# Kernel optimization log

Hardware: AMD Instinct MI355X
Metric: run time of the kernel (lower is better)

## Reference

```python
import jax, jax.numpy as jnp
import numpy as np

B, T, XS, HS = 256, 512, 256, 256


def setup_inputs() -> dict:
    key = jax.random.key(0)
    ks = jax.random.split(key, 9)
    scale_x = np.sqrt(6.0 / (XS + HS)).astype(np.float32)  # xavier_uniform-like scale
    scale_h = np.sqrt(6.0 / (HS + HS)).astype(np.float32)
    d = {"x": jax.random.normal(ks[0], (B, T, XS), dtype=jnp.float32)}
    names = ["i", "f", "g", "o"]
    for n, kx, kh in zip(names, ks[1:5], ks[5:9]):
        d[f"wx_{n}"] = jax.random.uniform(kx, (XS, HS), jnp.float32, -scale_x, scale_x)
        d[f"wh_{n}"] = jax.random.uniform(kh, (HS, HS), jnp.float32, -scale_h, scale_h)
        d[f"bx_{n}"] = jnp.zeros((HS,), jnp.float32)
        d[f"bh_{n}"] = jnp.zeros((HS,), jnp.float32)
    return d


def reference(x, wx_i, bx_i, wh_i, bh_i, wx_f, bx_f, wh_f, bh_f,
              wx_g, bx_g, wh_g, bh_g, wx_o, bx_o, wh_o, bh_o):
    bs, ts, xs = x.shape
    hs = wx_i.shape[1]
    # Fuse the 4 input projections and 4 hidden projections into 2 GEMMs
    # (identical math to 8 separate matmuls).
    Wx = jnp.concatenate([wx_i, wx_f, wx_g, wx_o], axis=1)      # [xs, 4hs]
    Wh = jnp.concatenate([wh_i, wh_f, wh_g, wh_o], axis=1)      # [hs, 4hs]
    b = jnp.concatenate([bx_i + bh_i, bx_f + bh_f, bx_g + bh_g, bx_o + bh_o])

    # Precompute all input projections in one big GEMM: [bs, ts, 4hs]
    x_proj = jnp.einsum('btx,xg->btg', x, Wx) + b

    def step(carry, xt_proj):
        h, c = carry
        gates = xt_proj + h @ Wh                      # [bs, 4hs]
        i_t = jax.nn.sigmoid(gates[:, 0 * hs:1 * hs])
        f_t = jax.nn.sigmoid(gates[:, 1 * hs:2 * hs])
        g_t = jnp.tanh(gates[:, 2 * hs:3 * hs])
        o_t = jax.nn.sigmoid(gates[:, 3 * hs:4 * hs])
        c_new = f_t * c + i_t * g_t
        h_new = o_t * jnp.tanh(c_new)
        return (h_new, c_new), None

    h0 = jnp.zeros((bs, hs), x.dtype)
    c0 = jnp.zeros((bs, hs), x.dtype)
    (h_t, c_t), _ = jax.lax.scan(step, (h0, c0), jnp.swapaxes(x_proj, 0, 1))
    return (h_t, c_t)
```

## Files before the change

### kernel.cpp

```cpp
#include <hip/hip_runtime.h>
#include <hip/hip_bf16.h>

#define BB   256
#define TT   512
#define XSZ  256
#define HSZ  256
#define GLDSW 132

typedef __bf16 bf16_t;
typedef __attribute__((ext_vector_type(8))) __bf16 bf16x8;
typedef __attribute__((ext_vector_type(4))) float  f32x4;
typedef __attribute__((ext_vector_type(4))) unsigned uint4v;

__device__ __forceinline__ float sigmoidf_(float v) { return 1.0f / (1.0f + __expf(-v)); }
__device__ __forceinline__ float tanhf_(float v)    { return 1.0f - 2.0f / (1.0f + __expf(2.0f * v)); }

__global__ void prep_bias(const float* bx0, const float* bh0, const float* bx1, const float* bh1,
                          const float* bx2, const float* bh2, const float* bx3, const float* bh3,
                          float* bias) {
  const float* bxs[4] = {bx0, bx1, bx2, bx3};
  const float* bhs[4] = {bh0, bh1, bh2, bh3};
  int g = blockIdx.x, c = threadIdx.x;
  bias[g * 256 + c] = bxs[g][c] + bhs[g][c];
}

__global__ void prep_wtf(const float* wx0, const float* wh0, const float* wx1, const float* wh1,
                         const float* wx2, const float* wh2, const float* wx3, const float* wh3,
                         bf16_t* Wtf) {
  const float* whs[4] = {wh0, wh1, wh2, wh3};
  const float* wxs[4] = {wx0, wx1, wx2, wx3};
  int id = blockIdx.x * 256 + threadIdx.x;
  int L  = id & 63;
  int kt = (id >> 6) & 15;
  int w  = (id >> 10) & 7;
  int j  = (id >> 13) & 7;
  int sec = w >> 1, half = w & 1;
  int c   = j * 32 + half * 16 + (L & 15);
  int k0  = kt * 32 + (L >> 4) * 8;
  const float* src = (k0 < 256) ? (whs[sec] + (size_t)k0 * 256 + c)
                                : (wxs[sec] + (size_t)(k0 - 256) * 256 + c);
  bf16x8 v;
#pragma unroll
  for (int i = 0; i < 8; ++i) v[i] = (__bf16)src[(size_t)i * 256];
  reinterpret_cast<bf16x8*>(Wtf)[id] = v;
}

__global__ void prep_xbf(const float* __restrict__ x, bf16_t* __restrict__ xb) {
  size_t id = (size_t)blockIdx.x * 256 + threadIdx.x;
  const float* p = x + id * 8;
  f32x4 lo = *reinterpret_cast<const f32x4*>(p);
  f32x4 hi = *reinterpret_cast<const f32x4*>(p + 4);
  bf16x8 v;
#pragma unroll
  for (int i = 0; i < 4; ++i) { v[i] = (__bf16)lo[i]; v[i + 4] = (__bf16)hi[i]; }
  reinterpret_cast<bf16x8*>(xb)[id] = v;
}

template <bool XBF>
__global__ __launch_bounds__(512, 2)
void lstm_seq(const void* __restrict__ xsrc, const bf16_t* __restrict__ Wtf,
              const float* __restrict__ bias, unsigned* __restrict__ hseq,
              float* __restrict__ out)
{
  __shared__ __align__(16) char  bxlds[65536];
  __shared__ __align__(16) char  hxl[2][8192];
  __shared__ __align__(16) float glds[16 * GLDSW];

  const int tid  = threadIdx.x;
  const int w    = tid >> 6;
  const int lane = tid & 63;
  const int l15  = lane & 15, l4 = lane >> 4;
  const int bid  = blockIdx.x;
  const int g    = bid >> 3, j = bid & 7;
  const int b0   = g * 16;
  const int sec  = w >> 1, half = w & 1;
  const int C    = sec * 256 + j * 32 + half * 16 + l15;

  const float*  xf32 = (const float*)xsrc;
  const bf16_t* xbf  = (const bf16_t*)xsrc;

  const float bias_v = bias[C];

  const char* wbase = (const char*)Wtf + ((size_t)(j * 8 + w) * 16) * 1024 + lane * 16;
  bf16x8 Bh[8];
#pragma unroll
  for (int kt = 0; kt < 8; ++kt)
    Bh[kt] = *reinterpret_cast<const bf16x8*>(wbase + kt * 1024);
#pragma unroll
  for (int q = 0; q < 8; ++q) {
    bf16x8 v = *reinterpret_cast<const bf16x8*>(wbase + (8 + q) * 1024);
    *reinterpret_cast<bf16x8*>(bxlds + (w * 8 + q) * 1024 + lane * 16) = v;
  }
  __syncthreads();

  const int crow = tid >> 5;
  const int ccol = tid & 31;
  float cst = 0.f;

  f32x4 acc_x = {bias_v, bias_v, bias_v, bias_v};
#pragma unroll
  for (int k8 = 0; k8 < 8; ++k8) {
    bf16x8 a;
    if constexpr (XBF) {
      a = *reinterpret_cast<const bf16x8*>(
          xbf + (size_t)(b0 + l15) * (TT * XSZ) + k8 * 32 + l4 * 8);
    } else {
      const float* xp = xf32 + (size_t)(b0 + l15) * (TT * XSZ) + k8 * 32 + l4 * 8;
      f32x4 lo = *reinterpret_cast<const f32x4*>(xp);
      f32x4 hi = *reinterpret_cast<const f32x4*>(xp + 4);
#pragma unroll
      for (int i = 0; i < 4; ++i) { a[i] = (__bf16)lo[i]; a[i + 4] = (__bf16)hi[i]; }
    }
    bf16x8 bx = *reinterpret_cast<const bf16x8*>(bxlds + (w * 8 + k8) * 1024 + lane * 16);
    acc_x = __builtin_amdgcn_mfma_f32_16x16x32_bf16(a, bx, acc_x, 0, 0, 0);
  }

#pragma unroll 1
  for (int t = 0; t < TT; ++t) {
    f32x4 acc = acc_x;

    bf16x8 ax[8];
    if constexpr (XBF) {
      if (t + 1 < TT) {
#pragma unroll
        for (int k8 = 0; k8 < 8; ++k8)
          ax[k8] = *reinterpret_cast<const bf16x8*>(
              xbf + (size_t)(b0 + l15) * (TT * XSZ) + (size_t)(t + 1) * XSZ + k8 * 32 + l4 * 8);
      }
    }

    if (t > 0) {
      const unsigned* hp = hseq + (size_t)(t & 1) * 65536
                         + (size_t)(b0 + l15) * HSZ + w * 32 + l4 * 8;
      const unsigned tg = (unsigned)t;
      uint4v A, B;
      for (;;) {
        asm volatile("global_load_dwordx4 %0, %2, off sc0 sc1\n\t"
                     "global_load_dwordx4 %1, %2, off offset:16 sc0 sc1\n\t"
                     "s_waitcnt vmcnt(0)"
                     : "=&v"(A), "=&v"(B) : "v"(hp) : "memory");
        bool ok = ((A[0] >> 16) == tg) & ((A[1] >> 16) == tg) &
                  ((A[2] >> 16) == tg) & ((A[3] >> 16) == tg) &
                  ((B[0] >> 16) == tg) & ((B[1] >> 16) == tg) &
                  ((B[2] >> 16) == tg) & ((B[3] >> 16) == tg);
        if (__all((int)ok)) break;
        __builtin_amdgcn_s_sleep(1);
      }
      __builtin_amdgcn_sched_barrier(0);
      unsigned p0 = (A[0] & 0xFFFFu) | (A[1] << 16);
      unsigned p1 = (A[2] & 0xFFFFu) | (A[3] << 16);
      unsigned p2 = (B[0] & 0xFFFFu) | (B[1] << 16);
      unsigned p3 = (B[2] & 0xFFFFu) | (B[3] << 16);
      uint4v pk = {p0, p1, p2, p3};
      *reinterpret_cast<uint4v*>(hxl[t & 1] + w * 1024 + lane * 16) = pk;
    }
    __syncthreads();

    if (t > 0) {
#pragma unroll
      for (int kt = 0; kt < 8; ++kt) {
        bf16x8 a = *reinterpret_cast<const bf16x8*>(hxl[t & 1] + kt * 1024 + lane * 16);
        acc = __builtin_amdgcn_mfma_f32_16x16x32_bf16(a, Bh[kt], acc, 0, 0, 0);
      }
    }

    {
      const int col = sec * 32 + half * 16 + l15;
#pragma unroll
      for (int r = 0; r < 4; ++r)
        glds[(l4 * 4 + r) * GLDSW + col] = acc[r];
    }
    __syncthreads();

    const float* gp = &glds[crow * GLDSW + ccol];
    float i_t = sigmoidf_(gp[0]);
    float f_t = sigmoidf_(gp[32]);
    float g_t = tanhf_(gp[64]);
    float o_t = sigmoidf_(gp[96]);
    float cn  = f_t * cst + i_t * g_t;
    cst = cn;
    float hval = o_t * tanhf_(cn);

    if (t + 1 < TT) {
      __bf16 hb16 = (__bf16)hval;
      unsigned hv = ((unsigned)(t + 1) << 16)
                  | (unsigned)__builtin_bit_cast(unsigned short, hb16);
      unsigned* hp = hseq + (size_t)((t + 1) & 1) * 65536
                   + (size_t)(b0 + crow) * HSZ + j * 32 + ccol;
      asm volatile("global_store_dword %0, %1, off sc0 sc1" :: "v"(hp), "v"(hv) : "memory");

      acc_x = f32x4{bias_v, bias_v, bias_v, bias_v};
#pragma unroll
      for (int k8 = 0; k8 < 8; ++k8) {
        bf16x8 a;
        if constexpr (XBF) {
          a = ax[k8];
        } else {
          const float* xp = xf32 + (size_t)(b0 + l15) * (TT * XSZ)
                          + (size_t)(t + 1) * XSZ + k8 * 32 + l4 * 8;
          f32x4 lo = *reinterpret_cast<const f32x4*>(xp);
          f32x4 hi = *reinterpret_cast<const f32x4*>(xp + 4);
#pragma unroll
          for (int i = 0; i < 4; ++i) { a[i] = (__bf16)lo[i]; a[i + 4] = (__bf16)hi[i]; }
        }
        bf16x8 bx = *reinterpret_cast<const bf16x8*>(bxlds + (w * 8 + k8) * 1024 + lane * 16);
        acc_x = __builtin_amdgcn_mfma_f32_16x16x32_bf16(a, bx, acc_x, 0, 0, 0);
      }
    } else {
      float* op = out + (size_t)(b0 + crow) * HSZ + j * 32 + ccol;
      op[0] = hval;
      op[(size_t)BB * HSZ] = cst;
    }
  }
}

extern "C" void kernel_launch(void* const* d_in, const int* in_sizes, int n_in,
                              void* d_out, int out_size, void* d_ws, size_t ws_size,
                              hipStream_t stream) {
  const float* x = (const float*)d_in[0];
  const float *wx[4], *wh[4], *bx[4], *bh[4];
  for (int g = 0; g < 4; ++g) {
    wx[g] = (const float*)d_in[1 + 4 * g];
    wh[g] = (const float*)d_in[2 + 4 * g];
    bx[g] = (const float*)d_in[3 + 4 * g];
    bh[g] = (const float*)d_in[4 + 4 * g];
  }

  char* ws = (char*)d_ws;
  float*    bias = (float*)ws;
  bf16_t*   Wtf  = (bf16_t*)(ws + 4096);
  unsigned* hseq = (unsigned*)(ws + 4096 + 1048576);
  bf16_t*   xbf  = (bf16_t*)(ws + 4096 + 1048576 + 524288);
  const size_t need_xbf = 4096 + 1048576 + 524288 + (size_t)BB * TT * XSZ * 2;

  prep_bias<<<dim3(4), dim3(256), 0, stream>>>(bx[0], bh[0], bx[1], bh[1],
                                               bx[2], bh[2], bx[3], bh[3], bias);
  prep_wtf<<<dim3(256), dim3(256), 0, stream>>>(wx[0], wh[0], wx[1], wh[1],
                                                wx[2], wh[2], wx[3], wh[3], Wtf);
  if (ws_size >= need_xbf) {
    prep_xbf<<<dim3((BB * TT * XSZ / 8) / 256), dim3(256), 0, stream>>>(x, xbf);
    lstm_seq<true><<<dim3(128), dim3(512), 0, stream>>>(xbf, Wtf, bias, hseq,
                                                        (float*)d_out);
  } else {
    lstm_seq<false><<<dim3(128), dim3(512), 0, stream>>>(x, Wtf, bias, hseq,
                                                         (float*)d_out);
  }
}
```

Baseline: 1.861 ms.

## Interleave gate columns so cell update runs in registers via lane shuffles

Reorders the fused weight layout so each group of four adjacent MFMA output columns holds the i/f/g/o gates of one hidden unit. The gate combination and cell update then run directly from the accumulators using lane shuffles, removing the LDS gate staging buffer and one block-wide barrier per timestep. Each wave now computes two N-tiles with all Wh and Wx fragments held in registers, so the grid halves to 64 blocks and the LDS copy of Wx goes away. The trade-offs are much higher register pressure, fewer blocks taking part in the recurrence, and the dropped prefetch of the next x step.

After: 2.227 ms. 1.2x slower.

```diff
diff --git a/kernel.cpp b/kernel.cpp
--- a/kernel.cpp
+++ b/kernel.cpp
@@ -5,15 +5,13 @@
 #define TT   512
 #define XSZ  256
 #define HSZ  256
-#define GLDSW 132
 
 typedef __bf16 bf16_t;
 typedef __attribute__((ext_vector_type(8))) __bf16 bf16x8;
 typedef __attribute__((ext_vector_type(4))) float  f32x4;
 typedef __attribute__((ext_vector_type(4))) unsigned uint4v;
 
-__device__ __forceinline__ float sigmoidf_(float v) { return 1.0f / (1.0f + __expf(-v)); }
-__device__ __forceinline__ float tanhf_(float v)    { return 1.0f - 2.0f / (1.0f + __expf(2.0f * v)); }
+__device__ __forceinline__ f32x4 splat4(float v) { f32x4 r = {v, v, v, v}; return r; }
 
 __global__ void prep_bias(const float* bx0, const float* bh0, const float* bx1, const float* bh1,
                           const float* bx2, const float* bh2, const float* bx3, const float* bh3,
@@ -32,13 +30,15 @@
   int id = blockIdx.x * 256 + threadIdx.x;
   int L  = id & 63;
   int kt = (id >> 6) & 15;
-  int w  = (id >> 10) & 7;
-  int j  = (id >> 13) & 7;
-  int sec = w >> 1, half = w & 1;
-  int c   = j * 32 + half * 16 + (L & 15);
-  int k0  = kt * 32 + (L >> 4) * 8;
-  const float* src = (k0 < 256) ? (whs[sec] + (size_t)k0 * 256 + c)
-                                : (wxs[sec] + (size_t)(k0 - 256) * 256 + c);
+  int nt = (id >> 10) & 1;
+  int w  = (id >> 11) & 7;
+  int j  = (id >> 14) & 3;
+  int tc   = L & 15;
+  int gate = tc & 3;
+  int hc   = j * 64 + w * 8 + nt * 4 + (tc >> 2);
+  int k0   = kt * 32 + (L >> 4) * 8;
+  const float* src = (k0 < 256) ? (whs[gate] + (size_t)k0 * 256 + hc)
+                                : (wxs[gate] + (size_t)(k0 - 256) * 256 + hc);
   bf16x8 v;
 #pragma unroll
   for (int i = 0; i < 8; ++i) v[i] = (__bf16)src[(size_t)i * 256];
@@ -62,42 +62,42 @@
               const float* __restrict__ bias, unsigned* __restrict__ hseq,
               float* __restrict__ out)
 {
-  __shared__ __align__(16) char  bxlds[65536];
-  __shared__ __align__(16) char  hxl[2][8192];
-  __shared__ __align__(16) float glds[16 * GLDSW];
+  __shared__ __align__(16) char hxl[2][8192];
 
   const int tid  = threadIdx.x;
   const int w    = tid >> 6;
   const int lane = tid & 63;
   const int l15  = lane & 15, l4 = lane >> 4;
   const int bid  = blockIdx.x;
-  const int g    = bid >> 3, j = bid & 7;
+  const int g    = bid >> 2, j = bid & 3;
   const int b0   = g * 16;
-  const int sec  = w >> 1, half = w & 1;
-  const int C    = sec * 256 + j * 32 + half * 16 + l15;
+  const int gate = l15 & 3;
+  const int hcg  = l15 >> 2;
+  const bool isg = (gate == 2);
 
   const float*  xf32 = (const float*)xsrc;
   const bf16_t* xbf  = (const bf16_t*)xsrc;
 
-  const float bias_v = bias[C];
-
-  const char* wbase = (const char*)Wtf + ((size_t)(j * 8 + w) * 16) * 1024 + lane * 16;
-  bf16x8 Bh[8];
-#pragma unroll
-  for (int kt = 0; kt < 8; ++kt)
-    Bh[kt] = *reinterpret_cast<const bf16x8*>(wbase + kt * 1024);
-#pragma unroll
-  for (int q = 0; q < 8; ++q) {
-    bf16x8 v = *reinterpret_cast<const bf16x8*>(wbase + (8 + q) * 1024);
-    *reinterpret_cast<bf16x8*>(bxlds + (w * 8 + q) * 1024 + lane * 16) = v;
-  }
-  __syncthreads();
-
-  const int crow = tid >> 5;
-  const int ccol = tid & 31;
-  float cst = 0.f;
-
-  f32x4 acc_x = {bias_v, bias_v, bias_v, bias_v};
+  const char* wbase = (const char*)Wtf + (size_t)(j * 256 + w * 32) * 1024 + lane * 16;
+  bf16x8 Bh[2][8], Bx[2][8];
+#pragma unroll
+  for (int nt = 0; nt < 2; ++nt)
+#pragma unroll
+    for (int kt = 0; kt < 8; ++kt) {
+      Bh[nt][kt] = *reinterpret_cast<const bf16x8*>(wbase + (nt * 16 + kt) * 1024);
+      Bx[nt][kt] = *reinterpret_cast<const bf16x8*>(wbase + (nt * 16 + 8 + kt) * 1024);
+    }
+
+  float bias_v[2];
+#pragma unroll
+  for (int nt = 0; nt < 2; ++nt)
+    bias_v[nt] = bias[gate * 256 + j * 64 + w * 8 + nt * 4 + hcg];
+
+  f32x4 cst0 = {0.f, 0.f, 0.f, 0.f};
+  f32x4 cst1 = {0.f, 0.f, 0.f, 0.f};
+
+  f32x4 acc_x0 = splat4(bias_v[0]);
+  f32x4 acc_x1 = splat4(bias_v[1]);
 #pragma unroll
   for (int k8 = 0; k8 < 8; ++k8) {
     bf16x8 a;
@@ -111,23 +111,14 @@
 #pragma unroll
       for (int i = 0; i < 4; ++i) { a[i] = (__bf16)lo[i]; a[i + 4] = (__bf16)hi[i]; }
     }
-    bf16x8 bx = *reinterpret_cast<const bf16x8*>(bxlds + (w * 8 + k8) * 1024 + lane * 16);
-    acc_x = __builtin_amdgcn_mfma_f32_16x16x32_bf16(a, bx, acc_x, 0, 0, 0);
+    acc_x0 = __builtin_amdgcn_mfma_f32_16x16x32_bf16(a, Bx[0][k8], acc_x0, 0, 0, 0);
+    acc_x1 = __builtin_amdgcn_mfma_f32_16x16x32_bf16(a, Bx[1][k8], acc_x1, 0, 0, 0);
   }
 
 #pragma unroll 1
   for (int t = 0; t < TT; ++t) {
-    f32x4 acc = acc_x;
-
-    bf16x8 ax[8];
-    if constexpr (XBF) {
-      if (t + 1 < TT) {
-#pragma unroll
-        for (int k8 = 0; k8 < 8; ++k8)
-          ax[k8] = *reinterpret_cast<const bf16x8*>(
-              xbf + (size_t)(b0 + l15) * (TT * XSZ) + (size_t)(t + 1) * XSZ + k8 * 32 + l4 * 8);
-      }
-    }
+    f32x4 acc0 = acc_x0;
+    f32x4 acc1 = acc_x1;
 
     if (t > 0) {
       const unsigned* hp = hseq + (size_t)(t & 1) * 65536
@@ -160,41 +151,72 @@
 #pragma unroll
       for (int kt = 0; kt < 8; ++kt) {
         bf16x8 a = *reinterpret_cast<const bf16x8*>(hxl[t & 1] + kt * 1024 + lane * 16);
-        acc = __builtin_amdgcn_mfma_f32_16x16x32_bf16(a, Bh[kt], acc, 0, 0, 0);
-      }
-    }
-
-    {
-      const int col = sec * 32 + half * 16 + l15;
-#pragma unroll
-      for (int r = 0; r < 4; ++r)
-        glds[(l4 * 4 + r) * GLDSW + col] = acc[r];
-    }
-    __syncthreads();
-
-    const float* gp = &glds[crow * GLDSW + ccol];
-    float i_t = sigmoidf_(gp[0]);
-    float f_t = sigmoidf_(gp[32]);
-    float g_t = tanhf_(gp[64]);
-    float o_t = sigmoidf_(gp[96]);
-    float cn  = f_t * cst + i_t * g_t;
-    cst = cn;
-    float hval = o_t * tanhf_(cn);
+        acc0 = __builtin_amdgcn_mfma_f32_16x16x32_bf16(a, Bh[0][kt], acc0, 0, 0, 0);
+        acc1 = __builtin_amdgcn_mfma_f32_16x16x32_bf16(a, Bh[1][kt], acc1, 0, 0, 0);
+      }
+    }
+
+    float hsel[2], csel[2];
+#pragma unroll
+    for (int nt = 0; nt < 2; ++nt) {
+      f32x4 acc = nt ? acc1 : acc0;
+      f32x4 av;
+#pragma unroll
+      for (int r = 0; r < 4; ++r) {
+        float p = isg ? 2.f * acc[r] : acc[r];
+        float s = 1.f / (1.f + __expf(-p));
+        av[r] = isg ? (2.f * s - 1.f) : s;
+      }
+      f32x4 bv, v0, v1, c0, c1;
+#pragma unroll
+      for (int r = 0; r < 4; ++r) bv[r] = __shfl_xor(av[r], 1);
+#pragma unroll
+      for (int r = 0; r < 4; ++r) {
+        v0[r] = (gate & 1) ? bv[r] : av[r];
+        v1[r] = (gate & 1) ? av[r] : bv[r];
+      }
+#pragma unroll
+      for (int r = 0; r < 4; ++r) { c0[r] = __shfl_xor(v0[r], 2); c1[r] = __shfl_xor(v1[r], 2); }
+      f32x4 hv;
+      f32x4 cs = nt ? cst1 : cst0;
+#pragma unroll
+      for (int r = 0; r < 4; ++r) {
+        float iv = (gate & 2) ? c0[r] : v0[r];
+        float fv = (gate & 2) ? c1[r] : v1[r];
+        float gv = (gate & 2) ? v0[r] : c0[r];
+        float ov = (gate & 2) ? v1[r] : c1[r];
+        float cn = fv * cs[r] + iv * gv;
+        cs[r] = cn;
+        float s2 = 1.f / (1.f + __expf(-2.f * cn));
+        hv[r] = ov * (2.f * s2 - 1.f);
+      }
+      if (nt) cst1 = cs; else cst0 = cs;
+      float hs = (gate == 0) ? hv[0] : (gate == 1) ? hv[1] : (gate == 2) ? hv[2] : hv[3];
+      float cc = (gate == 0) ? cs[0] : (gate == 1) ? cs[1] : (gate == 2) ? cs[2] : cs[3];
+      hsel[nt] = hs;
+      csel[nt] = cc;
+    }
 
     if (t + 1 < TT) {
-      __bf16 hb16 = (__bf16)hval;
-      unsigned hv = ((unsigned)(t + 1) << 16)
-                  | (unsigned)__builtin_bit_cast(unsigned short, hb16);
-      unsigned* hp = hseq + (size_t)((t + 1) & 1) * 65536
-                   + (size_t)(b0 + crow) * HSZ + j * 32 + ccol;
-      asm volatile("global_store_dword %0, %1, off sc0 sc1" :: "v"(hp), "v"(hv) : "memory");
-
-      acc_x = f32x4{bias_v, bias_v, bias_v, bias_v};
+#pragma unroll
+      for (int nt = 0; nt < 2; ++nt) {
+        __bf16 hb16 = (__bf16)hsel[nt];
+        unsigned hv = ((unsigned)(t + 1) << 16)
+                    | (unsigned)__builtin_bit_cast(unsigned short, hb16);
+        unsigned* hp2 = hseq + (size_t)((t + 1) & 1) * 65536
+                      + (size_t)(b0 + l4 * 4 + gate) * HSZ
+                      + (j * 64 + w * 8 + nt * 4 + hcg);
+        asm volatile("global_store_dword %0, %1, off sc0 sc1" :: "v"(hp2), "v"(hv) : "memory");
+      }
+
+      acc_x0 = splat4(bias_v[0]);
+      acc_x1 = splat4(bias_v[1]);
 #pragma unroll
       for (int k8 = 0; k8 < 8; ++k8) {
         bf16x8 a;
         if constexpr (XBF) {
-          a = ax[k8];
+          a = *reinterpret_cast<const bf16x8*>(
+              xbf + (size_t)(b0 + l15) * (TT * XSZ) + (size_t)(t + 1) * XSZ + k8 * 32 + l4 * 8);
         } else {
           const float* xp = xf32 + (size_t)(b0 + l15) * (TT * XSZ)
                           + (size_t)(t + 1) * XSZ + k8 * 32 + l4 * 8;
@@ -203,13 +225,17 @@
 #pragma unroll
           for (int i = 0; i < 4; ++i) { a[i] = (__bf16)lo[i]; a[i + 4] = (__bf16)hi[i]; }
         }
-        bf16x8 bx = *reinterpret_cast<const bf16x8*>(bxlds + (w * 8 + k8) * 1024 + lane * 16);
-        acc_x = __builtin_amdgcn_mfma_f32_16x16x32_bf16(a, bx, acc_x, 0, 0, 0);
+        acc_x0 = __builtin_amdgcn_mfma_f32_16x16x32_bf16(a, Bx[0][k8], acc_x0, 0, 0, 0);
+        acc_x1 = __builtin_amdgcn_mfma_f32_16x16x32_bf16(a, Bx[1][k8], acc_x1, 0, 0, 0);
       }
     } else {
-      float* op = out + (size_t)(b0 + crow) * HSZ + j * 32 + ccol;
-      op[0] = hval;
-      op[(size_t)BB * HSZ] = cst;
+#pragma unroll
+      for (int nt = 0; nt < 2; ++nt) {
+        float* op = out + (size_t)(b0 + l4 * 4 + gate) * HSZ
+                  + (j * 64 + w * 8 + nt * 4 + hcg);
+        op[0] = hsel[nt];
+        op[(size_t)BB * HSZ] = csel[nt];
+      }
     }
   }
 }
@@ -239,10 +265,10 @@
                                                 wx[2], wh[2], wx[3], wh[3], Wtf);
   if (ws_size >= need_xbf) {
     prep_xbf<<<dim3((BB * TT * XSZ / 8) / 256), dim3(256), 0, stream>>>(x, xbf);
-    lstm_seq<true><<<dim3(128), dim3(512), 0, stream>>>(xbf, Wtf, bias, hseq,
+    lstm_seq<true><<<dim3(64), dim3(512), 0, stream>>>(xbf, Wtf, bias, hseq,
+                                                       (float*)d_out);
+  } else {
+    lstm_seq<false><<<dim3(64), dim3(512), 0, stream>>>(x, Wtf, bias, hseq,
                                                         (float*)d_out);
-  } else {
-    lstm_seq<false><<<dim3(128), dim3(512), 0, stream>>>(x, Wtf, bias, hseq,
-                                                         (float*)d_out);
-  }
-}
+  }
+}
```
